# Optimization experiments

Measured on AMD Instinct MI355X. Metric: run time of the kernel, lower is better.

## Reference

```python
import jax, jax.numpy as jnp
import numpy as np

B, T, E, D = 64, 512, 1024, 1024  # batch, enc timesteps, enc hidden, dec hidden


def setup_inputs() -> dict:
    key = jax.random.key(0)
    ks = jax.random.split(key, 9)
    s = lambda fan_in: 1.0 / np.sqrt(fan_in)
    return {
        "hidden": jax.random.normal(ks[0], (B, D), jnp.float32),
        "decoder_out": jax.random.normal(ks[1], (B, D), jnp.float32),
        "encoder_states": jax.random.normal(ks[2], (T, B, E), jnp.float32),
        # attn: Linear(D+E -> 2E)
        "Wa": jax.random.uniform(ks[3], (2 * E, D + E), jnp.float32, -s(D + E), s(D + E)),
        "ba": jax.random.uniform(ks[4], (2 * E,), jnp.float32, -s(D + E), s(D + E)),
        # attn2: Linear(2E -> 1)
        "w2": jax.random.uniform(ks[5], (1, 2 * E), jnp.float32, -s(2 * E), s(2 * E)),
        "b2": jax.random.uniform(ks[6], (1,), jnp.float32, -s(2 * E), s(2 * E)),
        # attn_combine: Linear(D+E -> D)
        "Wc": jax.random.uniform(ks[7], (D, D + E), jnp.float32, -s(D + E), s(D + E)),
        "bc": jax.random.uniform(ks[8], (D,), jnp.float32, -s(D + E), s(D + E)),
    }


def reference(hidden, decoder_out, encoder_states, Wa, ba, w2, b2, Wc, bc):
    d = hidden.shape[1]
    # attn(cat(hidden, enc_t)) = hidden @ Wa[:, :D].T + enc_t @ Wa[:, D:].T + ba
    h_proj = hidden @ Wa[:, :d].T + ba                      # [B, 2E]
    e_proj = jnp.einsum('tbe,fe->tbf', encoder_states, Wa[:, d:])  # [T, B, 2E]
    act = jnp.tanh(h_proj[None, :, :] + e_proj)             # [T, B, 2E]
    scores = jnp.einsum('tbf,f->bt', act, w2[0]) + b2[0]    # [B, T]
    weights = jax.nn.softmax(scores, axis=-1)               # softmax over timesteps
    # weighted sum of encoder states: [B, E]
    applied = jnp.einsum('bt,tbe->be', weights, encoder_states)
    combined = jnp.concatenate([decoder_out, applied], axis=1)  # [B, D+E]
    out = jnp.tanh(combined @ Wc.T + bc)                    # [B, D]
    return out, applied
```

## Files before the change

### kernel.cpp

```cpp
#include <hip/hip_runtime.h>
#include <hip/hip_bf16.h>

#define BB 64
#define TT 512
#define EE 1024
#define DD 1024
#define BK 64

typedef __attribute__((ext_vector_type(8))) short s16x8;
typedef __attribute__((ext_vector_type(4))) float f32x4;

__device__ __forceinline__ float bf2f(unsigned short u) {
    unsigned int x = ((unsigned int)u) << 16;
    return __builtin_bit_cast(float, x);
}
__device__ __forceinline__ unsigned short f2bf(float f) {
    unsigned int u = __builtin_bit_cast(unsigned int, f);
    u += 0x7FFF + ((u >> 16) & 1);
    return (unsigned short)(u >> 16);
}
__device__ __forceinline__ float tanh_fast(float x) {
    x = fminf(fmaxf(x, -15.f), 15.f);
    float e = __expf(2.f * x);
    return (e - 1.f) / (e + 1.f);
}

__device__ __forceinline__ int tile_slot(int row, int g) {
    return (row >> 4) * 128 + (g >> 2) * 64 + (g & 3) * 16 + (row & 15);
}

__global__ __launch_bounds__(256) void conv_encS_kernel(
    const float* __restrict__ enc, unsigned short* __restrict__ encS)
{
    __shared__ short tileL[1024 * 8];
    const int tm  = blockIdx.x;
    const int tk  = blockIdx.y;
    const int tid = threadIdx.x;

#pragma unroll
    for (int it = 0; it < 4; ++it) {
        int cidx = it * 256 + tid;
        int row  = cidx >> 3;
        int g    = cidx & 7;
        const float* src = enc + (size_t)(tm * 128 + row) * 1024 + tk * 64 + g * 8;
        float4 v0 = ((const float4*)src)[0];
        float4 v1 = ((const float4*)src)[1];
        short c[8];
        c[0] = (short)f2bf(v0.x); c[1] = (short)f2bf(v0.y);
        c[2] = (short)f2bf(v0.z); c[3] = (short)f2bf(v0.w);
        c[4] = (short)f2bf(v1.x); c[5] = (short)f2bf(v1.y);
        c[6] = (short)f2bf(v1.z); c[7] = (short)f2bf(v1.w);
        *(s16x8*)&tileL[tile_slot(row, g) * 8] = *(s16x8*)c;
    }
    __syncthreads();
    unsigned short* dst = encS + ((size_t)tm * 16 + tk) * 8192;
#pragma unroll
    for (int it = 0; it < 4; ++it) {
        int s = it * 256 + tid;
        *(s16x8*)&dst[s * 8] = *(const s16x8*)&tileL[s * 8];
    }
}

__global__ __launch_bounds__(256) void conv_waS_kernel(
    const float* __restrict__ Wa, unsigned short* __restrict__ WaS)
{
    __shared__ short tileL[1024 * 8];
    const int tn  = blockIdx.x;
    const int tk  = blockIdx.y;
    const int tid = threadIdx.x;

#pragma unroll
    for (int it = 0; it < 4; ++it) {
        int cidx = it * 256 + tid;
        int row  = cidx >> 3;
        int g    = cidx & 7;
        const float* src = Wa + (size_t)(tn * 128 + row) * 2048 + 1024 + tk * 64 + g * 8;
        float4 v0 = ((const float4*)src)[0];
        float4 v1 = ((const float4*)src)[1];
        short c[8];
        c[0] = (short)f2bf(v0.x); c[1] = (short)f2bf(v0.y);
        c[2] = (short)f2bf(v0.z); c[3] = (short)f2bf(v0.w);
        c[4] = (short)f2bf(v1.x); c[5] = (short)f2bf(v1.y);
        c[6] = (short)f2bf(v1.z); c[7] = (short)f2bf(v1.w);
        *(s16x8*)&tileL[tile_slot(row, g) * 8] = *(s16x8*)c;
    }
    __syncthreads();
    unsigned short* dst = WaS + ((size_t)tn * 16 + tk) * 8192;
#pragma unroll
    for (int it = 0; it < 4; ++it) {
        int s = it * 256 + tid;
        *(s16x8*)&dst[s * 8] = *(const s16x8*)&tileL[s * 8];
    }
}

__global__ __launch_bounds__(256) void hproj_kernel(
    const float* __restrict__ hidden,
    const float* __restrict__ Wa,
    const float* __restrict__ ba,
    float* __restrict__ hp)
{
    __shared__ float sW[8 * 1024];
    const int tid  = threadIdx.x;
    const int lane = tid & 63;
    const int wave = tid >> 6;
    const int f0   = blockIdx.x * 8;

#pragma unroll
    for (int i = 0; i < 8; ++i) {
        int idx = i * 256 + tid;
        int fi  = idx >> 8;
        int c4  = idx & 255;
        ((float4*)sW)[idx] = *(const float4*)(Wa + (size_t)(f0 + fi) * 2048 + c4 * 4);
    }
    __syncthreads();

    for (int bi = 0; bi < 16; ++bi) {
        int b = wave * 16 + bi;
        float h[16];
#pragma unroll
        for (int j = 0; j < 16; ++j) h[j] = hidden[b * 1024 + lane + 64 * j];
#pragma unroll
        for (int fi = 0; fi < 8; ++fi) {
            float s = 0.f;
#pragma unroll
            for (int j = 0; j < 16; ++j) s += h[j] * sW[fi * 1024 + lane + 64 * j];
#pragma unroll
            for (int m = 32; m; m >>= 1) s += __shfl_xor(s, m);
            if (lane == 0) hp[(f0 + fi) * 64 + b] = s + ba[f0 + fi];
        }
    }
}

__global__ __launch_bounds__(256) void gemm_scores(
    const unsigned short* __restrict__ encS,
    const unsigned short* __restrict__ WaS,
    const float* __restrict__ hp,
    const float* __restrict__ w2,
    float* __restrict__ scores)
{
    __shared__ short sA[128 * BK];
    __shared__ short sB[128 * BK];
    __shared__ float rowAcc[128];

    const int tid  = threadIdx.x;
    const int bm   = blockIdx.x;
    const int bn   = blockIdx.y;
    const int lane = tid & 63;
    const int wave = tid >> 6;
    const int wm   = wave >> 1;
    const int wn   = wave & 1;
    const int c    = lane & 15;
    const int quad = lane >> 4;

    f32x4 acc[4][4];
#pragma unroll
    for (int mi = 0; mi < 4; ++mi)
#pragma unroll
        for (int ni = 0; ni < 4; ++ni)
#pragma unroll
            for (int r = 0; r < 4; ++r) acc[mi][ni][r] = 0.f;

    for (int kt = 0; kt < 16; ++kt) {
        const unsigned short* at = encS + ((size_t)bm * 16 + kt) * 8192;
        const unsigned short* bt = WaS  + ((size_t)bn * 16 + kt) * 8192;
#pragma unroll
        for (int i = 0; i < 4; ++i) {
            int s = i * 256 + tid;
            __builtin_amdgcn_global_load_lds(
                (const __attribute__((address_space(1))) void*)(at + s * 8),
                (__attribute__((address_space(3))) void*)&sA[s * 8], 16, 0, 0);
            __builtin_amdgcn_global_load_lds(
                (const __attribute__((address_space(1))) void*)(bt + s * 8),
                (__attribute__((address_space(3))) void*)&sB[s * 8], 16, 0, 0);
        }
        __builtin_amdgcn_s_waitcnt(0);
        __syncthreads();

#pragma unroll
        for (int kk = 0; kk < 2; ++kk) {
            s16x8 aF[4], bF[4];
#pragma unroll
            for (int mi = 0; mi < 4; ++mi)
                aF[mi] = *(const s16x8*)&sA[((wm * 4 + mi) * 128 + kk * 64 + lane) * 8];
#pragma unroll
            for (int ni = 0; ni < 4; ++ni)
                bF[ni] = *(const s16x8*)&sB[((wn * 4 + ni) * 128 + kk * 64 + lane) * 8];

#pragma unroll
            for (int mi = 0; mi < 4; ++mi)
#pragma unroll
                for (int ni = 0; ni < 4; ++ni)
                    acc[mi][ni] = __builtin_amdgcn_mfma_f32_16x16x32_bf16(
                        aF[mi], bF[ni], acc[mi][ni], 0, 0, 0);
        }
        __syncthreads();
    }

    float w2v[4];
#pragma unroll
    for (int ni = 0; ni < 4; ++ni) w2v[ni] = w2[bn * 128 + wn * 64 + ni * 16 + c];

    if (tid < 128) rowAcc[tid] = 0.f;
    __syncthreads();

#pragma unroll
    for (int mi = 0; mi < 4; ++mi) {
        int lrow0 = wm * 64 + mi * 16 + quad * 4;
        int b0    = (bm * 128 + lrow0) & 63;
        f32x4 hp4[4];
#pragma unroll
        for (int ni = 0; ni < 4; ++ni)
            hp4[ni] = *(const f32x4*)&hp[(bn * 128 + wn * 64 + ni * 16 + c) * 64 + b0];
#pragma unroll
        for (int r = 0; r < 4; ++r) {
            float s = 0.f;
#pragma unroll
            for (int ni = 0; ni < 4; ++ni)
                s += tanh_fast(acc[mi][ni][r] + hp4[ni][r]) * w2v[ni];
            s += __shfl_xor(s, 1);
            s += __shfl_xor(s, 2);
            s += __shfl_xor(s, 4);
            s += __shfl_xor(s, 8);
            if (c == 0) atomicAdd(&rowAcc[lrow0 + r], s);
        }
    }
    __syncthreads();
    if (tid < 128) {
        int grow = bm * 128 + tid;
        int b = grow & 63;
        int t = grow >> 6;
        atomicAdd(&scores[b * TT + t], rowAcc[tid]);
    }
}

__global__ __launch_bounds__(256) void softmax_kernel(float* __restrict__ scores)
{
    __shared__ float wmax[4];
    __shared__ float wsum[4];
    const int b   = blockIdx.x;
    const int tid = threadIdx.x;
    float* row = scores + b * TT;

    float v0 = row[tid], v1 = row[tid + 256];
    float m = fmaxf(v0, v1);
#pragma unroll
    for (int s = 32; s; s >>= 1) m = fmaxf(m, __shfl_xor(m, s));
    if ((tid & 63) == 0) wmax[tid >> 6] = m;
    __syncthreads();
    m = fmaxf(fmaxf(wmax[0], wmax[1]), fmaxf(wmax[2], wmax[3]));

    float e0 = __expf(v0 - m), e1 = __expf(v1 - m);
    float s = e0 + e1;
#pragma unroll
    for (int t = 32; t; t >>= 1) s += __shfl_xor(s, t);
    if ((tid & 63) == 0) wsum[tid >> 6] = s;
    __syncthreads();
    float inv = 1.f / (wsum[0] + wsum[1] + wsum[2] + wsum[3]);
    row[tid]       = e0 * inv;
    row[tid + 256] = e1 * inv;
}

__global__ __launch_bounds__(256) void applied_part_kernel(
    const float* __restrict__ enc,
    const float* __restrict__ w,
    float* __restrict__ part)
{
    __shared__ float red[128 * 8];
    const int tc  = blockIdx.x;
    const int b   = blockIdx.y;
    const int tid = threadIdx.x;
    const int eo  = tid & 127;
    const int th  = tid >> 7;
    const int e0  = eo * 8;

    float a[8];
#pragma unroll
    for (int j = 0; j < 8; ++j) a[j] = 0.f;

    for (int it = 0; it < 16; ++it) {
        int t = tc * 32 + th * 16 + it;
        float wt = w[b * TT + t];
        const float* src = enc + ((size_t)(t * BB + b)) * EE + e0;
        float4 v0 = ((const float4*)src)[0];
        float4 v1 = ((const float4*)src)[1];
        a[0] += wt * v0.x; a[1] += wt * v0.y; a[2] += wt * v0.z; a[3] += wt * v0.w;
        a[4] += wt * v1.x; a[5] += wt * v1.y; a[6] += wt * v1.z; a[7] += wt * v1.w;
    }
    if (th == 1) {
#pragma unroll
        for (int j = 0; j < 8; ++j) red[eo * 8 + j] = a[j];
    }
    __syncthreads();
    if (th == 0) {
        float* dst = part + ((size_t)tc * 64 + b) * 1024 + e0;
#pragma unroll
        for (int j = 0; j < 8; ++j) dst[j] = a[j] + red[eo * 8 + j];
    }
}

__global__ __launch_bounds__(256) void applied_reduce_kernel(
    const float* __restrict__ part, float* __restrict__ out_applied)
{
    int idx = blockIdx.x * 256 + threadIdx.x;
    float s = 0.f;
#pragma unroll
    for (int tc = 0; tc < 16; ++tc) s += part[tc * 65536 + idx];
    out_applied[idx] = s;
}

__global__ __launch_bounds__(256) void combine_kernel(
    const float* __restrict__ dec,
    const float* applied,
    const float* __restrict__ Wc,
    const float* __restrict__ bc,
    float* out0)
{
    const int g    = blockIdx.x * 4 + (threadIdx.x >> 6);
    const int lane = threadIdx.x & 63;
    const int d    = g >> 6;
    const int b    = g & 63;

    const float4* wc4 = (const float4*)Wc + (size_t)d * 512;
    const float4* de4 = (const float4*)dec + (size_t)b * 256;
    const float4* ap4 = (const float4*)applied + (size_t)b * 256;

    float s = 0.f;
#pragma unroll
    for (int j = 0; j < 4; ++j) {
        float4 a = de4[j * 64 + lane];
        float4 wv = wc4[j * 64 + lane];
        s += a.x * wv.x + a.y * wv.y + a.z * wv.z + a.w * wv.w;
    }
#pragma unroll
    for (int j = 0; j < 4; ++j) {
        float4 a = ap4[j * 64 + lane];
        float4 wv = wc4[256 + j * 64 + lane];
        s += a.x * wv.x + a.y * wv.y + a.z * wv.z + a.w * wv.w;
    }
#pragma unroll
    for (int m = 32; m; m >>= 1) s += __shfl_xor(s, m);
    if (lane == 0) out0[b * DD + d] = tanh_fast(s + bc[d]);
}

extern "C" void kernel_launch(void* const* d_in, const int* in_sizes, int n_in,
                              void* d_out, int out_size, void* d_ws, size_t ws_size,
                              hipStream_t stream) {
    const float* hidden = (const float*)d_in[0];
    const float* dec    = (const float*)d_in[1];
    const float* enc    = (const float*)d_in[2];
    const float* Wa     = (const float*)d_in[3];
    const float* ba     = (const float*)d_in[4];
    const float* w2     = (const float*)d_in[5];
    const float* Wc     = (const float*)d_in[7];
    const float* bc     = (const float*)d_in[8];
    float* out = (float*)d_out;

    unsigned short* encS = (unsigned short*)d_ws;
    unsigned short* WaS  = encS + (size_t)33554432;
    float* hp     = (float*)(WaS + (size_t)2097152);
    float* scores = hp + 131072;
    float* part   = scores + 32768;

    hipMemsetAsync(scores, 0, BB * TT * sizeof(float), stream);
    dim3 gc(256, 16);
    conv_encS_kernel<<<gc, 256, 0, stream>>>(enc, encS);
    dim3 gw(16, 16);
    conv_waS_kernel<<<gw, 256, 0, stream>>>(Wa, WaS);
    hproj_kernel<<<256, 256, 0, stream>>>(hidden, Wa, ba, hp);
    dim3 g2(256, 16);
    gemm_scores<<<g2, 256, 0, stream>>>(encS, WaS, hp, w2, scores);
    softmax_kernel<<<BB, 256, 0, stream>>>(scores);
    dim3 g3(16, 64);
    applied_part_kernel<<<g3, 256, 0, stream>>>(enc, scores, part);
    applied_reduce_kernel<<<256, 256, 0, stream>>>(part, out + BB * DD);
    combine_kernel<<<16384, 256, 0, stream>>>(dec, out + BB * DD, Wc, bc, out);
}
```

Before: 546.6 us.

## Load MFMA fragments directly from pre-swizzled global memory, widen N tile, drop score atomics

The scores GEMM stops staging tiles through LDS. Each wave now reads bf16 fragments straight from the pre-swizzled global layout, with register double-buffering across 32 half-K steps, and the per-block N tile doubles to 256 (8 MFMA columns per wave) under launch_bounds(256,2). Score partials are written to per-N-block slices that the softmax kernel sums, which removes the global atomics and the memset. The conversion kernels also write swizzled tiles directly without an LDS round trip. The risks are higher register pressure and less data reuse, since operand tiles are no longer shared through LDS and each wave refetches them from L2.

```diff
diff --git a/kernel.cpp b/kernel.cpp
--- a/kernel.cpp
+++ b/kernel.cpp
@@ -5,7 +5,6 @@
 #define TT 512
 #define EE 1024
 #define DD 1024
-#define BK 64
 
 typedef __attribute__((ext_vector_type(8))) short s16x8;
 typedef __attribute__((ext_vector_type(4))) float f32x4;
@@ -32,10 +31,10 @@
 __global__ __launch_bounds__(256) void conv_encS_kernel(
     const float* __restrict__ enc, unsigned short* __restrict__ encS)
 {
-    __shared__ short tileL[1024 * 8];
     const int tm  = blockIdx.x;
     const int tk  = blockIdx.y;
     const int tid = threadIdx.x;
+    unsigned short* dst = encS + ((size_t)tm * 16 + tk) * 8192;
 
 #pragma unroll
     for (int it = 0; it < 4; ++it) {
@@ -50,24 +49,17 @@
         c[2] = (short)f2bf(v0.z); c[3] = (short)f2bf(v0.w);
         c[4] = (short)f2bf(v1.x); c[5] = (short)f2bf(v1.y);
         c[6] = (short)f2bf(v1.z); c[7] = (short)f2bf(v1.w);
-        *(s16x8*)&tileL[tile_slot(row, g) * 8] = *(s16x8*)c;
-    }
-    __syncthreads();
-    unsigned short* dst = encS + ((size_t)tm * 16 + tk) * 8192;
-#pragma unroll
-    for (int it = 0; it < 4; ++it) {
-        int s = it * 256 + tid;
-        *(s16x8*)&dst[s * 8] = *(const s16x8*)&tileL[s * 8];
+        *(s16x8*)&dst[tile_slot(row, g) * 8] = *(s16x8*)c;
     }
 }
 
 __global__ __launch_bounds__(256) void conv_waS_kernel(
     const float* __restrict__ Wa, unsigned short* __restrict__ WaS)
 {
-    __shared__ short tileL[1024 * 8];
     const int tn  = blockIdx.x;
     const int tk  = blockIdx.y;
     const int tid = threadIdx.x;
+    unsigned short* dst = WaS + ((size_t)tn * 16 + tk) * 8192;
 
 #pragma unroll
     for (int it = 0; it < 4; ++it) {
@@ -82,14 +74,7 @@
         c[2] = (short)f2bf(v0.z); c[3] = (short)f2bf(v0.w);
         c[4] = (short)f2bf(v1.x); c[5] = (short)f2bf(v1.y);
         c[6] = (short)f2bf(v1.z); c[7] = (short)f2bf(v1.w);
-        *(s16x8*)&tileL[tile_slot(row, g) * 8] = *(s16x8*)c;
-    }
-    __syncthreads();
-    unsigned short* dst = WaS + ((size_t)tn * 16 + tk) * 8192;
-#pragma unroll
-    for (int it = 0; it < 4; ++it) {
-        int s = it * 256 + tid;
-        *(s16x8*)&dst[s * 8] = *(const s16x8*)&tileL[s * 8];
+        *(s16x8*)&dst[tile_slot(row, g) * 8] = *(s16x8*)c;
     }
 }
 
@@ -131,15 +116,13 @@
     }
 }
 
-__global__ __launch_bounds__(256) void gemm_scores(
+__global__ __launch_bounds__(256, 2) void gemm_scores(
     const unsigned short* __restrict__ encS,
     const unsigned short* __restrict__ WaS,
     const float* __restrict__ hp,
     const float* __restrict__ w2,
-    float* __restrict__ scores)
-{
-    __shared__ short sA[128 * BK];
-    __shared__ short sB[128 * BK];
+    float* __restrict__ scoresP)
+{
     __shared__ float rowAcc[128];
 
     const int tid  = threadIdx.x;
@@ -152,70 +135,71 @@
     const int c    = lane & 15;
     const int quad = lane >> 4;
 
-    f32x4 acc[4][4];
+    if (tid < 128) rowAcc[tid] = 0.f;
+
+    f32x4 acc[4][8];
 #pragma unroll
     for (int mi = 0; mi < 4; ++mi)
 #pragma unroll
-        for (int ni = 0; ni < 4; ++ni)
+        for (int ni = 0; ni < 8; ++ni)
 #pragma unroll
             for (int r = 0; r < 4; ++r) acc[mi][ni][r] = 0.f;
 
-    for (int kt = 0; kt < 16; ++kt) {
-        const unsigned short* at = encS + ((size_t)bm * 16 + kt) * 8192;
-        const unsigned short* bt = WaS  + ((size_t)bn * 16 + kt) * 8192;
-#pragma unroll
-        for (int i = 0; i < 4; ++i) {
-            int s = i * 256 + tid;
-            __builtin_amdgcn_global_load_lds(
-                (const __attribute__((address_space(1))) void*)(at + s * 8),
-                (__attribute__((address_space(3))) void*)&sA[s * 8], 16, 0, 0);
-            __builtin_amdgcn_global_load_lds(
-                (const __attribute__((address_space(1))) void*)(bt + s * 8),
-                (__attribute__((address_space(3))) void*)&sB[s * 8], 16, 0, 0);
+    const unsigned short* aBase = encS + (size_t)bm * 16 * 8192 + wm * 4096 + lane * 8;
+    const unsigned short* bBase = WaS + ((size_t)(bn * 2 + wn) * 16) * 8192 + lane * 8;
+
+    s16x8 aF[2][4], bF[2][8];
+
+#pragma unroll
+    for (int mi = 0; mi < 4; ++mi)
+        aF[0][mi] = *(const s16x8*)(aBase + mi * 1024);
+#pragma unroll
+    for (int ni = 0; ni < 8; ++ni)
+        bF[0][ni] = *(const s16x8*)(bBase + ni * 1024);
+
+#pragma unroll
+    for (int h = 0; h < 32; ++h) {
+        const int cur = h & 1;
+        const int nxt = cur ^ 1;
+        if (h < 31) {
+            const int h1 = h + 1;
+            const unsigned short* pa = aBase + (h1 >> 1) * 8192 + (h1 & 1) * 512;
+            const unsigned short* pb = bBase + (h1 >> 1) * 8192 + (h1 & 1) * 512;
+#pragma unroll
+            for (int mi = 0; mi < 4; ++mi)
+                aF[nxt][mi] = *(const s16x8*)(pa + mi * 1024);
+#pragma unroll
+            for (int ni = 0; ni < 8; ++ni)
+                bF[nxt][ni] = *(const s16x8*)(pb + ni * 1024);
         }
-        __builtin_amdgcn_s_waitcnt(0);
-        __syncthreads();
-
-#pragma unroll
-        for (int kk = 0; kk < 2; ++kk) {
-            s16x8 aF[4], bF[4];
-#pragma unroll
-            for (int mi = 0; mi < 4; ++mi)
-                aF[mi] = *(const s16x8*)&sA[((wm * 4 + mi) * 128 + kk * 64 + lane) * 8];
-#pragma unroll
-            for (int ni = 0; ni < 4; ++ni)
-                bF[ni] = *(const s16x8*)&sB[((wn * 4 + ni) * 128 + kk * 64 + lane) * 8];
-
-#pragma unroll
-            for (int mi = 0; mi < 4; ++mi)
-#pragma unroll
-                for (int ni = 0; ni < 4; ++ni)
-                    acc[mi][ni] = __builtin_amdgcn_mfma_f32_16x16x32_bf16(
-                        aF[mi], bF[ni], acc[mi][ni], 0, 0, 0);
-        }
-        __syncthreads();
-    }
-
-    float w2v[4];
-#pragma unroll
-    for (int ni = 0; ni < 4; ++ni) w2v[ni] = w2[bn * 128 + wn * 64 + ni * 16 + c];
-
-    if (tid < 128) rowAcc[tid] = 0.f;
-    __syncthreads();
+#pragma unroll
+        for (int mi = 0; mi < 4; ++mi)
+#pragma unroll
+            for (int ni = 0; ni < 8; ++ni)
+                acc[mi][ni] = __builtin_amdgcn_mfma_f32_16x16x32_bf16(
+                    aF[cur][mi], bF[cur][ni], acc[mi][ni], 0, 0, 0);
+    }
+
+    __syncthreads();
+
+    float w2v[8];
+#pragma unroll
+    for (int ni = 0; ni < 8; ++ni)
+        w2v[ni] = w2[bn * 256 + wn * 128 + ni * 16 + c];
 
 #pragma unroll
     for (int mi = 0; mi < 4; ++mi) {
         int lrow0 = wm * 64 + mi * 16 + quad * 4;
         int b0    = (bm * 128 + lrow0) & 63;
-        f32x4 hp4[4];
-#pragma unroll
-        for (int ni = 0; ni < 4; ++ni)
-            hp4[ni] = *(const f32x4*)&hp[(bn * 128 + wn * 64 + ni * 16 + c) * 64 + b0];
+        f32x4 hp4[8];
+#pragma unroll
+        for (int ni = 0; ni < 8; ++ni)
+            hp4[ni] = *(const f32x4*)&hp[(bn * 256 + wn * 128 + ni * 16 + c) * 64 + b0];
 #pragma unroll
         for (int r = 0; r < 4; ++r) {
             float s = 0.f;
 #pragma unroll
-            for (int ni = 0; ni < 4; ++ni)
+            for (int ni = 0; ni < 8; ++ni)
                 s += tanh_fast(acc[mi][ni][r] + hp4[ni][r]) * w2v[ni];
             s += __shfl_xor(s, 1);
             s += __shfl_xor(s, 2);
@@ -229,19 +213,25 @@
         int grow = bm * 128 + tid;
         int b = grow & 63;
         int t = grow >> 6;
-        atomicAdd(&scores[b * TT + t], rowAcc[tid]);
-    }
-}
-
-__global__ __launch_bounds__(256) void softmax_kernel(float* __restrict__ scores)
+        scoresP[((size_t)bn * 64 + b) * 512 + t] = rowAcc[tid];
+    }
+}
+
+__global__ __launch_bounds__(256) void softmax_kernel(
+    const float* __restrict__ scoresP, float* __restrict__ weights)
 {
     __shared__ float wmax[4];
     __shared__ float wsum[4];
     const int b   = blockIdx.x;
     const int tid = threadIdx.x;
-    float* row = scores + b * TT;
-
-    float v0 = row[tid], v1 = row[tid + 256];
+
+    float v0 = 0.f, v1 = 0.f;
+#pragma unroll
+    for (int p = 0; p < 8; ++p) {
+        const float* row = scoresP + ((size_t)p * 64 + b) * 512;
+        v0 += row[tid];
+        v1 += row[tid + 256];
+    }
     float m = fmaxf(v0, v1);
 #pragma unroll
     for (int s = 32; s; s >>= 1) m = fmaxf(m, __shfl_xor(m, s));
@@ -256,6 +246,7 @@
     if ((tid & 63) == 0) wsum[tid >> 6] = s;
     __syncthreads();
     float inv = 1.f / (wsum[0] + wsum[1] + wsum[2] + wsum[3]);
+    float* row = weights + (size_t)b * 512;
     row[tid]       = e0 * inv;
     row[tid + 256] = e1 * inv;
 }
@@ -357,21 +348,21 @@
 
     unsigned short* encS = (unsigned short*)d_ws;
     unsigned short* WaS  = encS + (size_t)33554432;
-    float* hp     = (float*)(WaS + (size_t)2097152);
-    float* scores = hp + 131072;
-    float* part   = scores + 32768;
-
-    hipMemsetAsync(scores, 0, BB * TT * sizeof(float), stream);
+    float* hp      = (float*)(WaS + (size_t)2097152);
+    float* scoresP = hp + 131072;
+    float* weights = scoresP + 262144;
+    float* part    = weights + 32768;
+
     dim3 gc(256, 16);
     conv_encS_kernel<<<gc, 256, 0, stream>>>(enc, encS);
     dim3 gw(16, 16);
     conv_waS_kernel<<<gw, 256, 0, stream>>>(Wa, WaS);
     hproj_kernel<<<256, 256, 0, stream>>>(hidden, Wa, ba, hp);
-    dim3 g2(256, 16);
-    gemm_scores<<<g2, 256, 0, stream>>>(encS, WaS, hp, w2, scores);
-    softmax_kernel<<<BB, 256, 0, stream>>>(scores);
+    dim3 g2(256, 8);
+    gemm_scores<<<g2, 256, 0, stream>>>(encS, WaS, hp, w2, scoresP);
+    softmax_kernel<<<BB, 256, 0, stream>>>(scoresP, weights);
     dim3 g3(16, 64);
-    applied_part_kernel<<<g3, 256, 0, stream>>>(enc, scores, part);
+    applied_part_kernel<<<g3, 256, 0, stream>>>(enc, weights, part);
     applied_reduce_kernel<<<256, 256, 0, stream>>>(part, out + BB * DD);
     combine_kernel<<<16384, 256, 0, stream>>>(dec, out + BB * DD, Wc, bc, out);
 }
```

Result: slower. 571.1 us (+4.5%).
